# Performance work log

Measured on AMD Instinct MI355X. Metric: run time of the kernel, lower is better.

The kernel has to match this reference:

```python
import jax, jax.numpy as jnp
import numpy as np

D_IN = 1024
D_OUT = 1024
SEQ = 4096


def setup_inputs() -> dict:
    key = jax.random.key(0)
    k0, k1, k2, k3 = jax.random.split(key, 4)
    inputs = jax.random.normal(k0, (SEQ, D_IN), dtype=jnp.float32)
    # original uses torch.rand (uniform [0,1)) for weights
    W_q = jax.random.uniform(k1, (D_IN, D_OUT), dtype=jnp.float32)
    W_k = jax.random.uniform(k2, (D_IN, D_OUT), dtype=jnp.float32)
    W_v = jax.random.uniform(k3, (D_IN, D_OUT), dtype=jnp.float32)
    return {"inputs": inputs, "W_q": W_q, "W_k": W_k, "W_v": W_v}


def reference(inputs, W_q, W_k, W_v):
    queries = inputs @ W_q            # [S, d_out]
    keys = inputs @ W_k               # [S, d_out]
    values = inputs @ W_v             # [S, d_out]
    d_k = keys.shape[-1]
    scale = 1.0 / jnp.sqrt(jnp.asarray(d_k, dtype=queries.dtype))
    attn_scores = queries @ keys.T    # [S, S]
    attn_weights = jax.nn.softmax(attn_scores * scale, axis=-1)
    context_vectors = attn_weights @ values  # [S, d_out]
    return context_vectors
```

## Files before the change

kernel.cpp:

```cpp
#include <hip/hip_runtime.h>

typedef unsigned short u16;
typedef __attribute__((ext_vector_type(8))) short bf16x8;
typedef __attribute__((ext_vector_type(4))) float f32x4;

#define SEQ 4096
#define DIM 1024

__device__ __forceinline__ u16 f2bf(float f) {
  unsigned u = __float_as_uint(f);
  return (u16)((u + 0x7fffu + ((u >> 16) & 1u)) >> 16);
}
__device__ __forceinline__ float bf2f(u16 h) {
  return __uint_as_float(((unsigned)h) << 16);
}

__device__ __forceinline__ void gload_lds16(const void* g, void* l) {
  __builtin_amdgcn_global_load_lds(
      (const __attribute__((address_space(1))) void*)g,
      (__attribute__((address_space(3))) void*)l, 16, 0, 0);
}

__device__ __forceinline__ void stage_tile(const u16* __restrict__ g, int ld,
                                           u16* lds, int tid) {
  const int w = tid >> 6;
#pragma unroll
  for (int it = 0; it < 2; ++it) {
    int c = it * 256 + tid;
    int row = c >> 2, ch = c & 3;
    gload_lds16(g + (size_t)row * ld + ch * 8, lds + (size_t)(it * 256 + w * 64) * 8);
  }
}

template <int NPAIR>
__device__ __forceinline__ void gemm_multi(
    const u16* A0, const u16* A1,
    const u16* B0, const u16* B1,
    int K, int ldA, int ldB,
    u16* lds, f32x4 (&acc)[4][4]) {
  const int tid = threadIdx.x;
  const int w = tid >> 6, l = tid & 63;
  const int wm = w >> 1, wn = w & 1;
  const int lr = l & 15, q = l >> 4;
  u16* lA0 = lds;
  u16* lB0 = lds + 4096;
  u16* lA1 = lds + 8192;
  u16* lB1 = lds + 12288;

#pragma unroll
  for (int mi = 0; mi < 4; ++mi)
#pragma unroll
    for (int ni = 0; ni < 4; ++ni)
      acc[mi][ni] = (f32x4){0.f, 0.f, 0.f, 0.f};

  const int ao = (wm * 64 + lr) * 32 + q * 8;
  const int bo = (wn * 64 + lr) * 32 + q * 8;

  for (int k0 = 0; k0 < K; k0 += 32) {
    stage_tile(A0 + k0, ldA, lA0, tid);
    stage_tile(B0 + k0, ldB, lB0, tid);
    if constexpr (NPAIR >= 3) {
      stage_tile(A1 + k0, ldA, lA1, tid);
      stage_tile(B1 + k0, ldB, lB1, tid);
    }
    __syncthreads();
    bf16x8 a0[4], b0[4];
#pragma unroll
    for (int i = 0; i < 4; ++i) {
      a0[i] = *(const bf16x8*)(lA0 + ao + i * 512);
      b0[i] = *(const bf16x8*)(lB0 + bo + i * 512);
    }
#pragma unroll
    for (int mi = 0; mi < 4; ++mi)
#pragma unroll
      for (int ni = 0; ni < 4; ++ni)
        acc[mi][ni] = __builtin_amdgcn_mfma_f32_16x16x32_bf16(
            a0[mi], b0[ni], acc[mi][ni], 0, 0, 0);
    if constexpr (NPAIR >= 3) {
      bf16x8 b1[4];
#pragma unroll
      for (int i = 0; i < 4; ++i) b1[i] = *(const bf16x8*)(lB1 + bo + i * 512);
#pragma unroll
      for (int mi = 0; mi < 4; ++mi)
#pragma unroll
        for (int ni = 0; ni < 4; ++ni)
          acc[mi][ni] = __builtin_amdgcn_mfma_f32_16x16x32_bf16(
              a0[mi], b1[ni], acc[mi][ni], 0, 0, 0);
      bf16x8 a1[4];
#pragma unroll
      for (int i = 0; i < 4; ++i) a1[i] = *(const bf16x8*)(lA1 + ao + i * 512);
#pragma unroll
      for (int mi = 0; mi < 4; ++mi)
#pragma unroll
        for (int ni = 0; ni < 4; ++ni)
          acc[mi][ni] = __builtin_amdgcn_mfma_f32_16x16x32_bf16(
              a1[mi], b0[ni], acc[mi][ni], 0, 0, 0);
    }
    __syncthreads();
  }
}

#define EPILOGUE_IDX                                          \
  const int tid = threadIdx.x, w = tid >> 6, l = tid & 63;    \
  const int wm = w >> 1, wn = w & 1, lr = l & 15, q = l >> 4; \
  (void)tid;


__global__ __launch_bounds__(256) void split_x_kernel(const float* __restrict__ X,
                                                      u16* __restrict__ Xh,
                                                      u16* __restrict__ Xl) {
  int i = (blockIdx.x * 256 + threadIdx.x) * 4;
  float4 x = *(const float4*)(X + i);
  ushort4 h, lo;
  float v;
  v = x.x; h.x = f2bf(v); lo.x = f2bf(v - bf2f(h.x));
  v = x.y; h.y = f2bf(v); lo.y = f2bf(v - bf2f(h.y));
  v = x.z; h.z = f2bf(v); lo.z = f2bf(v - bf2f(h.z));
  v = x.w; h.w = f2bf(v); lo.w = f2bf(v - bf2f(h.w));
  *(ushort4*)(Xh + i) = h;
  *(ushort4*)(Xl + i) = lo;
}

__global__ __launch_bounds__(256) void split_w_t_kernel(
    const float* __restrict__ W0, const float* __restrict__ W1, const float* __restrict__ W2,
    u16* __restrict__ H0, u16* __restrict__ L0,
    u16* __restrict__ H1, u16* __restrict__ L1,
    u16* __restrict__ H2) {
  __shared__ float t[32][33];
  const int z = blockIdx.z;
  const float* W = (z == 0) ? W0 : (z == 1) ? W1 : W2;
  u16* H = (z == 0) ? H0 : (z == 1) ? H1 : H2;
  u16* L = (z == 0) ? L0 : (z == 1) ? L1 : nullptr;
  const int i0 = blockIdx.y * 32, o0 = blockIdx.x * 32;
  const int tx = threadIdx.x, ty = threadIdx.y;
#pragma unroll
  for (int m = 0; m < 4; ++m)
    t[ty + 8 * m][tx] = W[(size_t)(i0 + ty + 8 * m) * DIM + o0 + tx];
  __syncthreads();
#pragma unroll
  for (int m = 0; m < 4; ++m) {
    float v = t[tx][ty + 8 * m];
    u16 h = f2bf(v);
    size_t o = (size_t)(o0 + ty + 8 * m) * DIM + i0 + tx;
    H[o] = h;
    if (L) L[o] = f2bf(v - bf2f(h));
  }
}

__global__ __launch_bounds__(256) void qkv_kernel(
    const u16* __restrict__ Xh, const u16* __restrict__ Xl,
    const u16* __restrict__ Wh0, const u16* __restrict__ Wl0,
    const u16* __restrict__ Wh1, const u16* __restrict__ Wl1,
    const u16* __restrict__ Wh2,
    u16* __restrict__ Qh, u16* __restrict__ Ql,
    u16* __restrict__ Kh, u16* __restrict__ Kl,
    u16* __restrict__ VT) {
  __shared__ __align__(16) u16 lds[4 * 4096];
  const int z = blockIdx.z;
  f32x4 acc[4][4];
  if (z < 2) {
    const u16* Wh = z ? Wh1 : Wh0;
    const u16* Wl = z ? Wl1 : Wl0;
    const int row0 = blockIdx.y * 128, col0 = blockIdx.x * 128;
    gemm_multi<3>(Xh + (size_t)row0 * DIM, Xl + (size_t)row0 * DIM,
                  Wh + (size_t)col0 * DIM, Wl + (size_t)col0 * DIM,
                  DIM, DIM, DIM, lds, acc);
    EPILOGUE_IDX
    u16* H = z ? Kh : Qh;
    u16* L = z ? Kl : Ql;
#pragma unroll
    for (int mi = 0; mi < 4; ++mi)
#pragma unroll
      for (int ni = 0; ni < 4; ++ni)
#pragma unroll
        for (int r = 0; r < 4; ++r) {
          int row = row0 + wm * 64 + mi * 16 + q * 4 + r;
          int col = col0 + wn * 64 + ni * 16 + lr;
          float v = acc[mi][ni][r];
          u16 h = f2bf(v);
          size_t o = (size_t)row * DIM + col;
          H[o] = h;
          L[o] = f2bf(v - bf2f(h));
        }
  } else {
    const int row0 = blockIdx.x * 128;
    const int col0 = blockIdx.y * 128;
    gemm_multi<1>(Wh2 + (size_t)row0 * DIM, nullptr,
                  Xh + (size_t)col0 * DIM, nullptr,
                  DIM, DIM, DIM, lds, acc);
    EPILOGUE_IDX
#pragma unroll
    for (int mi = 0; mi < 4; ++mi)
#pragma unroll
      for (int ni = 0; ni < 4; ++ni)
#pragma unroll
        for (int r = 0; r < 4; ++r) {
          int row = row0 + wm * 64 + mi * 16 + q * 4 + r;
          int col = col0 + wn * 64 + ni * 16 + lr;
          VT[(size_t)row * SEQ + col] = f2bf(acc[mi][ni][r]);
        }
  }
}

__global__ __launch_bounds__(256) void s_kernel(
    const u16* __restrict__ Qh, const u16* __restrict__ Ql,
    const u16* __restrict__ Kh, const u16* __restrict__ Kl,
    float* __restrict__ S) {
  __shared__ __align__(16) u16 lds[4 * 4096];
  const int row0 = blockIdx.y * 128, col0 = blockIdx.x * 128;
  f32x4 acc[4][4];
  gemm_multi<3>(Qh + (size_t)row0 * DIM, Ql + (size_t)row0 * DIM,
                Kh + (size_t)col0 * DIM, Kl + (size_t)col0 * DIM,
                DIM, DIM, DIM, lds, acc);
  EPILOGUE_IDX
  const float scale = 0.03125f;
#pragma unroll
  for (int mi = 0; mi < 4; ++mi)
#pragma unroll
    for (int ni = 0; ni < 4; ++ni)
#pragma unroll
      for (int r = 0; r < 4; ++r) {
        int row = row0 + wm * 64 + mi * 16 + q * 4 + r;
        int col = col0 + wn * 64 + ni * 16 + lr;
        S[(size_t)row * SEQ + col] = acc[mi][ni][r] * scale;
      }
}

__global__ __launch_bounds__(256) void softmax_kernel(const float* __restrict__ S,
                                                      u16* __restrict__ P) {
  const int row = blockIdx.x;
  const float* s = S + (size_t)row * SEQ;
  const int tid = threadIdx.x;
  float v[16];
  float mx = -3.4e38f;
#pragma unroll
  for (int i = 0; i < 16; ++i) {
    v[i] = s[tid + i * 256];
    mx = fmaxf(mx, v[i]);
  }
#pragma unroll
  for (int off = 32; off; off >>= 1) mx = fmaxf(mx, __shfl_xor(mx, off));
  __shared__ float red[8];
  const int w = tid >> 6, l = tid & 63;
  if (l == 0) red[w] = mx;
  __syncthreads();
  mx = fmaxf(fmaxf(red[0], red[1]), fmaxf(red[2], red[3]));
  float sum = 0.f;
#pragma unroll
  for (int i = 0; i < 16; ++i) {
    v[i] = __expf(v[i] - mx);
    sum += v[i];
  }
#pragma unroll
  for (int off = 32; off; off >>= 1) sum += __shfl_xor(sum, off);
  if (l == 0) red[4 + w] = sum;
  __syncthreads();
  sum = red[4] + red[5] + red[6] + red[7];
  const float inv = 1.f / sum;
  u16* p = P + (size_t)row * SEQ;
#pragma unroll
  for (int i = 0; i < 16; ++i) p[tid + i * 256] = f2bf(v[i] * inv);
}

__global__ __launch_bounds__(256) void o_kernel(const u16* __restrict__ P,
                                                const u16* __restrict__ VT,
                                                float* __restrict__ Opart) {
  __shared__ __align__(16) u16 lds[2 * 4096];
  const int z = blockIdx.z;
  const int row0 = blockIdx.y * 128, col0 = blockIdx.x * 128;
  const u16* A = P + (size_t)row0 * SEQ + z * 1024;
  const u16* B = VT + (size_t)col0 * SEQ + z * 1024;
  f32x4 acc[4][4];
  gemm_multi<1>(A, nullptr, B, nullptr, 1024, SEQ, SEQ, lds, acc);
  EPILOGUE_IDX
  float* O = Opart + (size_t)z * SEQ * DIM;
#pragma unroll
  for (int mi = 0; mi < 4; ++mi)
#pragma unroll
    for (int ni = 0; ni < 4; ++ni)
#pragma unroll
      for (int r = 0; r < 4; ++r) {
        int row = row0 + wm * 64 + mi * 16 + q * 4 + r;
        int col = col0 + wn * 64 + ni * 16 + lr;
        O[(size_t)row * DIM + col] = acc[mi][ni][r];
      }
}

__global__ __launch_bounds__(256) void o_reduce_kernel(const float* __restrict__ Op,
                                                       float* __restrict__ O) {
  const size_t N = (size_t)SEQ * DIM;
  size_t i = ((size_t)blockIdx.x * 256 + threadIdx.x) * 4;
  float4 a = *(const float4*)(Op + i);
  float4 b = *(const float4*)(Op + N + i);
  float4 c = *(const float4*)(Op + 2 * N + i);
  float4 d = *(const float4*)(Op + 3 * N + i);
  float4 r;
  r.x = (a.x + b.x) + (c.x + d.x);
  r.y = (a.y + b.y) + (c.y + d.y);
  r.z = (a.z + b.z) + (c.z + d.z);
  r.w = (a.w + b.w) + (c.w + d.w);
  *(float4*)(O + i) = r;
}

extern "C" void kernel_launch(void* const* d_in, const int* in_sizes, int n_in,
                              void* d_out, int out_size, void* d_ws, size_t ws_size,
                              hipStream_t stream) {
  const float* X = (const float*)d_in[0];
  const float* Wq = (const float*)d_in[1];
  const float* Wk = (const float*)d_in[2];
  const float* Wv = (const float*)d_in[3];

  const size_t MB = 1024 * 1024;
  char* w = (char*)d_ws;
  u16* Xh = (u16*)(w + 0 * MB);
  u16* Xl = (u16*)(w + 8 * MB);
  u16* WqhT = (u16*)(w + 16 * MB);
  u16* WqlT = (u16*)(w + 18 * MB);
  u16* WkhT = (u16*)(w + 20 * MB);
  u16* WklT = (u16*)(w + 22 * MB);
  u16* WvhT = (u16*)(w + 24 * MB);
  u16* Qh = (u16*)(w + 26 * MB);
  u16* Ql = (u16*)(w + 34 * MB);
  u16* Kh = (u16*)(w + 42 * MB);
  u16* Kl = (u16*)(w + 50 * MB);
  u16* VT = (u16*)(w + 58 * MB);
  float* S = (float*)(w + 66 * MB);
  u16* P = (u16*)(w + 26 * MB);
  float* Opart = (float*)(w + 66 * MB);

  split_x_kernel<<<(SEQ * DIM) / (256 * 4), 256, 0, stream>>>(X, Xh, Xl);
  split_w_t_kernel<<<dim3(32, 32, 3), dim3(32, 8), 0, stream>>>(
      Wq, Wk, Wv, WqhT, WqlT, WkhT, WklT, WvhT);
  qkv_kernel<<<dim3(DIM / 128, SEQ / 128, 3), 256, 0, stream>>>(
      Xh, Xl, WqhT, WqlT, WkhT, WklT, WvhT, Qh, Ql, Kh, Kl, VT);
  s_kernel<<<dim3(SEQ / 128, SEQ / 128), 256, 0, stream>>>(Qh, Ql, Kh, Kl, S);
  softmax_kernel<<<SEQ, 256, 0, stream>>>(S, P);
  o_kernel<<<dim3(DIM / 128, SEQ / 128, 4), 256, 0, stream>>>(P, VT, Opart);
  o_reduce_kernel<<<(SEQ * DIM) / (256 * 4), 256, 0, stream>>>(Opart, (float*)d_out);
}
```

Measured before the change: 336.7 us.

## Reorder LDS staging layout for conflict-free MFMA reads and fuse prep kernels

The global-to-LDS staging now maps each 16-row by 8-column chunk group so that each lane's MFMA operand sits contiguously at lane*8 in LDS. The aim is to remove LDS bank conflicts on the fragment reads in every GEMM. Separately, the X split and the W transpose/split kernels are merged into one prep launch, with z=0 handling X, which saves one kernel launch. The global reads become less contiguous per row (16-byte chunks spread across rows), which could slightly hurt coalescing.

```diff
diff --git a/kernel.cpp b/kernel.cpp
--- a/kernel.cpp
+++ b/kernel.cpp
@@ -27,8 +27,9 @@
 #pragma unroll
   for (int it = 0; it < 2; ++it) {
     int c = it * 256 + tid;
-    int row = c >> 2, ch = c & 3;
-    gload_lds16(g + (size_t)row * ld + ch * 8, lds + (size_t)(it * 256 + w * 64) * 8);
+    int row = ((c >> 6) << 4) | (c & 15);
+    int gch = (c >> 4) & 3;
+    gload_lds16(g + (size_t)row * ld + gch * 8, lds + (size_t)(it * 256 + w * 64) * 8);
   }
 }
 
@@ -41,7 +42,6 @@
   const int tid = threadIdx.x;
   const int w = tid >> 6, l = tid & 63;
   const int wm = w >> 1, wn = w & 1;
-  const int lr = l & 15, q = l >> 4;
   u16* lA0 = lds;
   u16* lB0 = lds + 4096;
   u16* lA1 = lds + 8192;
@@ -53,8 +53,8 @@
     for (int ni = 0; ni < 4; ++ni)
       acc[mi][ni] = (f32x4){0.f, 0.f, 0.f, 0.f};
 
-  const int ao = (wm * 64 + lr) * 32 + q * 8;
-  const int bo = (wn * 64 + lr) * 32 + q * 8;
+  const int ao = wm * 2048 + l * 8;
+  const int bo = wn * 2048 + l * 8;
 
   for (int k0 = 0; k0 < K; k0 += 32) {
     stage_tile(A0 + k0, ldA, lA0, tid);
@@ -106,33 +106,38 @@
   (void)tid;
 
 
-__global__ __launch_bounds__(256) void split_x_kernel(const float* __restrict__ X,
-                                                      u16* __restrict__ Xh,
-                                                      u16* __restrict__ Xl) {
-  int i = (blockIdx.x * 256 + threadIdx.x) * 4;
-  float4 x = *(const float4*)(X + i);
-  ushort4 h, lo;
-  float v;
-  v = x.x; h.x = f2bf(v); lo.x = f2bf(v - bf2f(h.x));
-  v = x.y; h.y = f2bf(v); lo.y = f2bf(v - bf2f(h.y));
-  v = x.z; h.z = f2bf(v); lo.z = f2bf(v - bf2f(h.z));
-  v = x.w; h.w = f2bf(v); lo.w = f2bf(v - bf2f(h.w));
-  *(ushort4*)(Xh + i) = h;
-  *(ushort4*)(Xl + i) = lo;
-}
-
-__global__ __launch_bounds__(256) void split_w_t_kernel(
+__global__ __launch_bounds__(256) void prep_kernel(
+    const float* __restrict__ X,
     const float* __restrict__ W0, const float* __restrict__ W1, const float* __restrict__ W2,
+    u16* __restrict__ Xh, u16* __restrict__ Xl,
     u16* __restrict__ H0, u16* __restrict__ L0,
     u16* __restrict__ H1, u16* __restrict__ L1,
     u16* __restrict__ H2) {
+  const int z = blockIdx.z;
+  const int tx = threadIdx.x, ty = threadIdx.y;
+  if (z == 0) {
+    int idx = (blockIdx.y * 32 + blockIdx.x) * 256 + ty * 32 + tx;
+    int i0 = idx * 16;
+#pragma unroll
+    for (int j = 0; j < 4; ++j) {
+      int i = i0 + j * 4;
+      float4 x = *(const float4*)(X + i);
+      ushort4 h, lo;
+      float v;
+      v = x.x; h.x = f2bf(v); lo.x = f2bf(v - bf2f(h.x));
+      v = x.y; h.y = f2bf(v); lo.y = f2bf(v - bf2f(h.y));
+      v = x.z; h.z = f2bf(v); lo.z = f2bf(v - bf2f(h.z));
+      v = x.w; h.w = f2bf(v); lo.w = f2bf(v - bf2f(h.w));
+      *(ushort4*)(Xh + i) = h;
+      *(ushort4*)(Xl + i) = lo;
+    }
+    return;
+  }
   __shared__ float t[32][33];
-  const int z = blockIdx.z;
-  const float* W = (z == 0) ? W0 : (z == 1) ? W1 : W2;
-  u16* H = (z == 0) ? H0 : (z == 1) ? H1 : H2;
-  u16* L = (z == 0) ? L0 : (z == 1) ? L1 : nullptr;
+  const float* W = (z == 1) ? W0 : (z == 2) ? W1 : W2;
+  u16* H = (z == 1) ? H0 : (z == 2) ? H1 : H2;
+  u16* L = (z == 1) ? L0 : (z == 2) ? L1 : nullptr;
   const int i0 = blockIdx.y * 32, o0 = blockIdx.x * 32;
-  const int tx = threadIdx.x, ty = threadIdx.y;
 #pragma unroll
   for (int m = 0; m < 4; ++m)
     t[ty + 8 * m][tx] = W[(size_t)(i0 + ty + 8 * m) * DIM + o0 + tx];
@@ -328,9 +333,8 @@
   u16* P = (u16*)(w + 26 * MB);
   float* Opart = (float*)(w + 66 * MB);
 
-  split_x_kernel<<<(SEQ * DIM) / (256 * 4), 256, 0, stream>>>(X, Xh, Xl);
-  split_w_t_kernel<<<dim3(32, 32, 3), dim3(32, 8), 0, stream>>>(
-      Wq, Wk, Wv, WqhT, WqlT, WkhT, WklT, WvhT);
+  prep_kernel<<<dim3(32, 32, 4), dim3(32, 8), 0, stream>>>(
+      X, Wq, Wk, Wv, Xh, Xl, WqhT, WqlT, WkhT, WklT, WvhT);
   qkv_kernel<<<dim3(DIM / 128, SEQ / 128, 3), 256, 0, stream>>>(
       Xh, Xl, WqhT, WqlT, WkhT, WklT, WvhT, Qh, Ql, Kh, Kl, VT);
   s_kernel<<<dim3(SEQ / 128, SEQ / 128), 256, 0, stream>>>(Qh, Ql, Kh, Kl, S);
```

Result: slower. 399.3 us (+18.6%).
